# Performance work log

Measured on AMD Instinct MI355X. Metric: run time of the kernel, lower is better.

The kernel has to match this reference:

```python
import jax, jax.numpy as jnp
import numpy as np


def setup_inputs() -> dict:
    key = jax.random.key(0)
    k1, k2 = jax.random.split(key)
    attn = jax.random.normal(k1, (2, 16, 1024, 4096), dtype=jnp.float32)
    ref_target_masks = jax.random.randint(k2, (4, 4096), 0, 2, dtype=jnp.int32)
    return {"attn": attn, "ref_target_masks": ref_target_masks}


def reference(attn, ref_target_masks):
    # mode = 'mean' (default in the torch module)
    masks = ref_target_masks.astype(attn.dtype)            # (C, R)
    sm = jax.nn.softmax(attn, axis=-1)                     # (B, H, S, R)
    # per-class masked sum over ref tokens: (C, B, H, S)
    weighted = jnp.einsum('bhsr,cr->cbhs', sm, masks)
    # normalize by mask sum per class
    weighted = weighted / masks.sum(axis=-1)[:, None, None, None]
    # permute (B,H,S)->(B,S,H) then mean over heads -> (C, B, S)
    return weighted.mean(axis=2)
```

## Files before the change

kernel.cpp:

```cpp
#include <hip/hip_runtime.h>

static constexpr int R = 4096;
static constexpr int C = 4;
static constexpr int NH = 16;
static constexpr int S = 1024;
static constexpr int B = 2;
static constexpr int BLOCK = 256;
static constexpr int NWAVE = BLOCK / 64;

__global__ __launch_bounds__(BLOCK) void pack_masks_kernel(
    const int* __restrict__ masks, unsigned char* __restrict__ codes,
    float* __restrict__ scale) {
  __shared__ float red[NWAVE][C];
  const int t = threadIdx.x;
  int cnt[C] = {0, 0, 0, 0};
  for (int k = 0; k < R / BLOCK; ++k) {
    const int r = k * BLOCK + t;
    unsigned code = 0;
#pragma unroll
    for (int c = 0; c < C; ++c) {
      const int m = (masks[c * R + r] != 0);
      code |= (unsigned)m << c;
      cnt[c] += m;
    }
    codes[r] = (unsigned char)code;
  }
#pragma unroll
  for (int c = 0; c < C; ++c) {
    float v = (float)cnt[c];
#pragma unroll
    for (int off = 32; off; off >>= 1) v += __shfl_xor(v, off, 64);
    if ((t & 63) == 0) red[t >> 6][c] = v;
  }
  __syncthreads();
  if (t == 0) {
#pragma unroll
    for (int c = 0; c < C; ++c) {
      float tot = 0.f;
      for (int w = 0; w < NWAVE; ++w) tot += red[w][c];
      scale[c] = 1.0f / (tot * (float)NH);
    }
  }
}

__global__ __launch_bounds__(BLOCK, 4) void wave_rows_kernel(
    const float* __restrict__ attn, const unsigned* __restrict__ codes,
    const float* __restrict__ scale, float* __restrict__ out) {
  const int t = threadIdx.x;
  const int lane = t & 63;
  const int wid = t >> 6;
  const int wave = blockIdx.x * NWAVE + wid;
  const int bs = wave >> 2;
  const int hg = wave & 3;
  const int b = bs >> 10;
  const int s = bs & (S - 1);

  unsigned cw[16];
#pragma unroll
  for (int i = 0; i < 16; ++i) cw[i] = codes[i * 64 + lane];

  float res[C] = {0.f, 0.f, 0.f, 0.f};

#pragma unroll
  for (int hh = 0; hh < NH / 4; ++hh) {
    const int h = hg * 4 + hh;
    const size_t row = (size_t)(b * NH + h) * S + s;
    const float4* rp = reinterpret_cast<const float4*>(attn + row * R);

    float denom = 0.f;
    float num[C] = {0.f, 0.f, 0.f, 0.f};
#pragma unroll
    for (int i = 0; i < 16; ++i) {
      const float4 a = rp[i * 64 + lane];
      const unsigned w = cw[i];
      const float av[4] = {a.x, a.y, a.z, a.w};
#pragma unroll
      for (int e = 0; e < 4; ++e) {
        const float ex = __expf(av[e]);
        denom += ex;
        const unsigned cc = w >> (8 * e);
#pragma unroll
        for (int c = 0; c < C; ++c) num[c] += ((cc >> c) & 1u) ? ex : 0.f;
      }
    }

    float vals[5] = {denom, num[0], num[1], num[2], num[3]};
#pragma unroll
    for (int v = 0; v < 5; ++v) {
#pragma unroll
      for (int off = 32; off; off >>= 1) vals[v] += __shfl_xor(vals[v], off, 64);
    }
    const float invd = 1.0f / vals[0];
#pragma unroll
    for (int c = 0; c < C; ++c) res[c] += vals[1 + c] * invd;
  }

  if (lane == 0) {
    float* outp = out + b * S + s;
#pragma unroll
    for (int c = 0; c < C; ++c)
      atomicAdd(outp + c * (B * S), res[c] * scale[c]);
  }
}

__global__ __launch_bounds__(BLOCK) void row_fallback_kernel(
    const float* __restrict__ attn, const int* __restrict__ masks,
    float* __restrict__ out) {
  const int row = blockIdx.x;
  const int t = threadIdx.x;
  __shared__ unsigned lds_words[R / 4];
  __shared__ float red[NWAVE][9];

  float cntf[C] = {0.f, 0.f, 0.f, 0.f};
#pragma unroll
  for (int kw = 0; kw < R / 4 / BLOCK; ++kw) {
    const int j = kw * BLOCK + t;
    unsigned word = 0;
#pragma unroll
    for (int i = 0; i < 4; ++i) {
      const int r = 4 * j + i;
#pragma unroll
      for (int c = 0; c < C; ++c) {
        const int m = (masks[c * R + r] != 0);
        word |= (unsigned)m << (8 * i + c);
        cntf[c] += (float)m;
      }
    }
    lds_words[j] = word;
  }
  __syncthreads();

  const float4* rowp = reinterpret_cast<const float4*>(attn + (size_t)row * R);
  float denom = 0.f;
  float num[C] = {0.f, 0.f, 0.f, 0.f};
#pragma unroll
  for (int k = 0; k < R / 4 / BLOCK; ++k) {
    const int j = k * BLOCK + t;
    const float4 a = rowp[j];
    const unsigned w = lds_words[j];
    const float av[4] = {a.x, a.y, a.z, a.w};
#pragma unroll
    for (int i = 0; i < 4; ++i) {
      const float e = __expf(av[i]);
      denom += e;
      const unsigned cc = w >> (8 * i);
#pragma unroll
      for (int c = 0; c < C; ++c) num[c] += ((cc >> c) & 1u) ? e : 0.f;
    }
  }

  float vals[9] = {denom, num[0], num[1], num[2], num[3],
                   cntf[0], cntf[1], cntf[2], cntf[3]};
#pragma unroll
  for (int iv = 0; iv < 9; ++iv) {
#pragma unroll
    for (int off = 32; off; off >>= 1) vals[iv] += __shfl_xor(vals[iv], off, 64);
  }
  const int wave = t >> 6;
  if ((t & 63) == 0)
    for (int iv = 0; iv < 9; ++iv) red[wave][iv] = vals[iv];
  __syncthreads();
  if (t == 0) {
    float tot[9];
    for (int iv = 0; iv < 9; ++iv)
      tot[iv] = red[0][iv] + red[1][iv] + red[2][iv] + red[3][iv];
    const float inv_d = 1.0f / tot[0];
    const int s = row & (S - 1);
    const int b = row >> 14;
    float* outp = out + b * S + s;
#pragma unroll
    for (int c = 0; c < C; ++c)
      atomicAdd(outp + c * (B * S),
                tot[1 + c] * inv_d / (tot[5 + c] * (float)NH));
  }
}

extern "C" void kernel_launch(void* const* d_in, const int* in_sizes, int n_in,
                              void* d_out, int out_size, void* d_ws,
                              size_t ws_size, hipStream_t stream) {
  const float* attn = (const float*)d_in[0];
  const int* masks = (const int*)d_in[1];
  float* out = (float*)d_out;

  hipMemsetAsync(d_out, 0, (size_t)out_size * sizeof(float), stream);

  const size_t need = (size_t)R + C * sizeof(float);
  if (ws_size >= need) {
    unsigned char* codes = (unsigned char*)d_ws;
    float* scale = (float*)((char*)d_ws + R);
    pack_masks_kernel<<<1, BLOCK, 0, stream>>>(masks, codes, scale);
    const int waves = B * S * 4;
    wave_rows_kernel<<<waves / NWAVE, BLOCK, 0, stream>>>(
        attn, (const unsigned*)codes, scale, out);
  } else {
    row_fallback_kernel<<<B * NH * S, BLOCK, 0, stream>>>(attn, masks, out);
  }
}
```

Before: 709.3 us.

## Assign one wave per attention row and use bit-trick FMA masking

Each wave now processes a single (b,h,s) row instead of four heads, giving four times more waves and one atomic per row per class instead of one per four heads. Mask codes are reloaded from global memory (cached) per row rather than held in registers across heads. The select is replaced by building 2.0f from the mask bit and using an FMA, so the scale is halved to compensate. This adds more atomic traffic on the same output addresses in exchange for more parallelism and less register pressure.

```diff
diff --git a/kernel.cpp b/kernel.cpp
--- a/kernel.cpp
+++ b/kernel.cpp
@@ -38,68 +38,56 @@
     for (int c = 0; c < C; ++c) {
       float tot = 0.f;
       for (int w = 0; w < NWAVE; ++w) tot += red[w][c];
-      scale[c] = 1.0f / (tot * (float)NH);
+      scale[c] = 0.5f / (tot * (float)NH);
     }
   }
 }
 
-__global__ __launch_bounds__(BLOCK, 4) void wave_rows_kernel(
+__global__ __launch_bounds__(BLOCK, 4) void wave_row_kernel(
     const float* __restrict__ attn, const unsigned* __restrict__ codes,
     const float* __restrict__ scale, float* __restrict__ out) {
   const int t = threadIdx.x;
   const int lane = t & 63;
-  const int wid = t >> 6;
-  const int wave = blockIdx.x * NWAVE + wid;
-  const int bs = wave >> 2;
-  const int hg = wave & 3;
-  const int b = bs >> 10;
-  const int s = bs & (S - 1);
+  const int row = blockIdx.x * NWAVE + (t >> 6);
 
-  unsigned cw[16];
-#pragma unroll
-  for (int i = 0; i < 16; ++i) cw[i] = codes[i * 64 + lane];
+  const float4* rp = reinterpret_cast<const float4*>(attn + (size_t)row * R);
 
-  float res[C] = {0.f, 0.f, 0.f, 0.f};
+  float denom = 0.f;
+  float num[C] = {0.f, 0.f, 0.f, 0.f};
 
 #pragma unroll
-  for (int hh = 0; hh < NH / 4; ++hh) {
-    const int h = hg * 4 + hh;
-    const size_t row = (size_t)(b * NH + h) * S + s;
-    const float4* rp = reinterpret_cast<const float4*>(attn + row * R);
-
-    float denom = 0.f;
-    float num[C] = {0.f, 0.f, 0.f, 0.f};
+  for (int i = 0; i < 16; ++i) {
+    const float4 a = rp[i * 64 + lane];
+    const unsigned w = codes[i * 64 + lane];
+    const float av[4] = {a.x, a.y, a.z, a.w};
 #pragma unroll
-    for (int i = 0; i < 16; ++i) {
-      const float4 a = rp[i * 64 + lane];
-      const unsigned w = cw[i];
-      const float av[4] = {a.x, a.y, a.z, a.w};
+    for (int e = 0; e < 4; ++e) {
+      const float ex = __expf(av[e]);
+      denom += ex;
+      const unsigned cc = w >> (8 * e);
 #pragma unroll
-      for (int e = 0; e < 4; ++e) {
-        const float ex = __expf(av[e]);
-        denom += ex;
-        const unsigned cc = w >> (8 * e);
-#pragma unroll
-        for (int c = 0; c < C; ++c) num[c] += ((cc >> c) & 1u) ? ex : 0.f;
+      for (int c = 0; c < C; ++c) {
+        const unsigned bits = (cc << (30 - c)) & 0x40000000u;
+        num[c] = fmaf(__uint_as_float(bits), ex, num[c]);
       }
     }
+  }
 
-    float vals[5] = {denom, num[0], num[1], num[2], num[3]};
+  float vals[5] = {denom, num[0], num[1], num[2], num[3]};
 #pragma unroll
-    for (int v = 0; v < 5; ++v) {
+  for (int v = 0; v < 5; ++v) {
 #pragma unroll
-      for (int off = 32; off; off >>= 1) vals[v] += __shfl_xor(vals[v], off, 64);
-    }
-    const float invd = 1.0f / vals[0];
-#pragma unroll
-    for (int c = 0; c < C; ++c) res[c] += vals[1 + c] * invd;
+    for (int off = 32; off; off >>= 1) vals[v] += __shfl_xor(vals[v], off, 64);
   }
 
   if (lane == 0) {
+    const float invd = 1.0f / vals[0];
+    const int s = row & (S - 1);
+    const int b = row >> 14;
     float* outp = out + b * S + s;
 #pragma unroll
     for (int c = 0; c < C; ++c)
-      atomicAdd(outp + c * (B * S), res[c] * scale[c]);
+      atomicAdd(outp + c * (B * S), vals[1 + c] * invd * scale[c]);
   }
 }
 
@@ -189,8 +177,8 @@
     unsigned char* codes = (unsigned char*)d_ws;
     float* scale = (float*)((char*)d_ws + R);
     pack_masks_kernel<<<1, BLOCK, 0, stream>>>(masks, codes, scale);
-    const int waves = B * S * 4;
-    wave_rows_kernel<<<waves / NWAVE, BLOCK, 0, stream>>>(
+    const int rows = B * NH * S;
+    wave_row_kernel<<<rows / NWAVE, BLOCK, 0, stream>>>(
         attn, (const unsigned*)codes, scale, out);
   } else {
     row_fallback_kernel<<<B * NH * S, BLOCK, 0, stream>>>(attn, masks, out);
```

Result: faster. 674.5 us (-4.9%).
